# Kernel tuning notes

Measured on AMD Instinct MI355X. Metric: run time of the kernel, lower is better.

The kernel has to match this reference:

```python
import jax, jax.numpy as jnp
import numpy as np

D = 1024  # dim_context


def setup_inputs() -> dict:
    key = jax.random.key(0)
    k1, k2, k3, k4, k5 = jax.random.split(key, 5)
    B, T = 32, 2048
    hidden = jax.random.normal(k1, (B, D), dtype=jnp.float32)
    encoder_outputs = jax.random.normal(k2, (B, T, D), dtype=jnp.float32)
    # nn.Linear(2D, D): weight [D, 2D], bias [D]
    lim = 1.0 / np.sqrt(2 * D)
    W = jax.random.uniform(k3, (D, 2 * D), minval=-lim, maxval=lim, dtype=jnp.float32)
    b = jax.random.uniform(k4, (D,), minval=-lim, maxval=lim, dtype=jnp.float32)
    stdv = 1.0 / np.sqrt(D)
    v = jax.random.uniform(k5, (D,), minval=-stdv, maxval=stdv, dtype=jnp.float32)
    return {"hidden": hidden, "encoder_outputs": encoder_outputs, "W": W, "b": b, "v": v}


def reference(hidden, encoder_outputs, W, b, v):
    # hidden: [B, D]; encoder_outputs: [B, T, D]
    B, T, Dm = encoder_outputs.shape
    h = jnp.broadcast_to(hidden[:, None, :], (B, T, Dm))      # repeat over T
    attn_inputs = jnp.concatenate([h, encoder_outputs], axis=2)  # [B, T, 2D]
    energy = jax.nn.relu(jnp.einsum('btk,dk->btd', attn_inputs, W) + b)  # [B, T, D]
    scores = jnp.einsum('btd,d->bt', energy, v)                # [B, T]
    # softmax over dim=1 (time axis), then unsqueeze(1)
    return jax.nn.softmax(scores, axis=1)[:, None, :]          # [B, 1, T]
```

## Files before the change

### kernel.cpp

```cpp
#include <hip/hip_runtime.h>
#include <cstdint>


#define GLOBAL_AS __attribute__((address_space(1)))
#define LDS_AS    __attribute__((address_space(3)))

typedef __bf16 bf16x8 __attribute__((ext_vector_type(8)));
typedef float  f32x4  __attribute__((ext_vector_type(4)));

__device__ __forceinline__ unsigned int f2bf(float x) {
    unsigned int u = __builtin_bit_cast(unsigned int, x);
    u += 0x7fffu + ((u >> 16) & 1u);
    return u >> 16;
}

__global__ __launch_bounds__(256) void k_convert_enc(const float4* __restrict__ in,
                                                     uint4* __restrict__ out) {
    size_t idx = (size_t)blockIdx.x * 256 + threadIdx.x;
    float4 f0 = in[idx * 2];
    float4 f1 = in[idx * 2 + 1];
    uint4 o;
    o.x = f2bf(f0.x) | (f2bf(f0.y) << 16);
    o.y = f2bf(f0.z) | (f2bf(f0.w) << 16);
    o.z = f2bf(f1.x) | (f2bf(f1.y) << 16);
    o.w = f2bf(f1.z) | (f2bf(f1.w) << 16);
    out[idx] = o;
}

__global__ __launch_bounds__(256) void k_convert_we(const float* __restrict__ W,
                                                    uint2* __restrict__ out) {
    int idx = blockIdx.x * 256 + threadIdx.x;
    int i = idx * 4;
    int n = i >> 10, k = i & 1023;
    const float4 f = *(const float4*)(W + (size_t)n * 2048 + 1024 + k);
    uint2 o;
    o.x = f2bf(f.x) | (f2bf(f.y) << 16);
    o.y = f2bf(f.z) | (f2bf(f.w) << 16);
    out[idx] = o;
}

__global__ __launch_bounds__(256) void k_hidden_proj(const float* __restrict__ hidden,
                                                     const float* __restrict__ W,
                                                     const float* __restrict__ bias,
                                                     float* __restrict__ u) {
    __shared__ float wrow[1024];
    __shared__ float red[256];
    const int tid = threadIdx.x, d = blockIdx.x;
    ((float4*)wrow)[tid] = ((const float4*)(W + (size_t)d * 2048))[tid];
    __syncthreads();
    const int b = tid & 31, kc = tid >> 5;
    const float* h = hidden + b * 1024 + kc * 128;
    const float* w = wrow + kc * 128;
    float acc = 0.f;
    #pragma unroll 8
    for (int i = 0; i < 128; i += 4) {
        float4 hv = *(const float4*)(h + i);
        acc += w[i] * hv.x + w[i + 1] * hv.y + w[i + 2] * hv.z + w[i + 3] * hv.w;
    }
    red[tid] = acc;
    __syncthreads();
    if (tid < 32) {
        float s = 0.f;
        #pragma unroll
        for (int j = 0; j < 8; j++) s += red[j * 32 + tid];
        u[tid * 1024 + d] = s + bias[d];
    }
}


#define STAGE_A(S, h, kk) do {                                                          \
    __builtin_amdgcn_global_load_lds(                                                   \
        (GLOBAL_AS void*)(size_t)(Ab + arow0 + (kk) + (h) * 32),                        \
        (LDS_AS void*)(&As[S][h][c0 * 512]), 16, 0, 0);                                 \
    __builtin_amdgcn_global_load_lds(                                                   \
        (GLOBAL_AS void*)(size_t)(Ab + arow1 + (kk) + (h) * 32),                        \
        (LDS_AS void*)(&As[S][h][c0 * 512 + 512]), 16, 0, 0);                           \
} while (0)

#define STAGE_B(S, h, kk, nbn) do {                                                     \
    __builtin_amdgcn_global_load_lds(                                                   \
        (GLOBAL_AS void*)(size_t)(Bw + (size_t)(nbn) * 262144 + brow0 + (kk) + (h) * 32), \
        (LDS_AS void*)(&Bs[S][h][c0 * 512]), 16, 0, 0);                                 \
    __builtin_amdgcn_global_load_lds(                                                   \
        (GLOBAL_AS void*)(size_t)(Bw + (size_t)(nbn) * 262144 + brow1 + (kk) + (h) * 32), \
        (LDS_AS void*)(&Bs[S][h][c0 * 512 + 512]), 16, 0, 0);                           \
} while (0)

#define PHASE_MFMA(jp)                                                                  \
    __builtin_amdgcn_s_barrier();                                                       \
    asm volatile("s_waitcnt lgkmcnt(0)" ::: "memory");                                  \
    __builtin_amdgcn_sched_barrier(0);                                                  \
    __builtin_amdgcn_s_setprio(1);                                                      \
    _Pragma("unroll")                                                                   \
    for (int i = 0; i < 8; i++) {                                                       \
        acc[i][2 * (jp)]     = __builtin_amdgcn_mfma_f32_16x16x32_bf16(                 \
            afr[i], bfr[0], acc[i][2 * (jp)], 0, 0, 0);                                 \
        acc[i][2 * (jp) + 1] = __builtin_amdgcn_mfma_f32_16x16x32_bf16(                 \
            afr[i], bfr[1], acc[i][2 * (jp) + 1], 0, 0, 0);                             \
    }                                                                                   \
    __builtin_amdgcn_s_setprio(0);                                                      \
    __builtin_amdgcn_s_barrier();

#define TILE(C, S, kst, nbn) do {                                                       \
    {                                                               \
        const unsigned short* Ap = As[C][0];                                            \
        const unsigned short* Bp = Bs[C][0];                                            \
        _Pragma("unroll")                                                               \
        for (int i = 0; i < 8; i++) afr[i] = *(const bf16x8*)(Ap + aBase + i * 512);    \
        bfr[0] = *(const bf16x8*)(Bp + bBase);                                          \
        bfr[1] = *(const bf16x8*)(Bp + bBase + 512);                                    \
        STAGE_A(S, 0, kst);                                                             \
        PHASE_MFMA(0)                                                                   \
    }                                                                                   \
    {                                                               \
        const unsigned short* Bp = Bs[C][0];                                            \
        bfr[0] = *(const bf16x8*)(Bp + bBase + 1024);                                   \
        bfr[1] = *(const bf16x8*)(Bp + bBase + 1536);                                   \
        STAGE_B(S, 0, kst, nbn);                                                        \
        asm volatile("s_waitcnt vmcnt(4)" ::: "memory");                                \
        PHASE_MFMA(1)                                                                   \
    }                                                                                   \
    {                                                               \
        const unsigned short* Ap = As[C][1];                                            \
        const unsigned short* Bp = Bs[C][1];                                            \
        _Pragma("unroll")                                                               \
        for (int i = 0; i < 8; i++) afr[i] = *(const bf16x8*)(Ap + aBase + i * 512);    \
        bfr[0] = *(const bf16x8*)(Bp + bBase);                                          \
        bfr[1] = *(const bf16x8*)(Bp + bBase + 512);                                    \
        STAGE_A(S, 1, kst);                                                             \
        PHASE_MFMA(0)                                                                   \
    }                                                                                   \
    {                                                               \
        const unsigned short* Bp = Bs[C][1];                                            \
        bfr[0] = *(const bf16x8*)(Bp + bBase + 1024);                                   \
        bfr[1] = *(const bf16x8*)(Bp + bBase + 1536);                                   \
        STAGE_B(S, 1, kst, nbn);                                                        \
        asm volatile("s_waitcnt vmcnt(4)" ::: "memory");                                \
        PHASE_MFMA(1)                                                                   \
    }                                                                                   \
} while (0)

__global__ __launch_bounds__(512, 2) void k_gemm_score(
        const unsigned short* __restrict__ Ab,
        const unsigned short* __restrict__ Bw,
        const float* __restrict__ u,
        const float* __restrict__ v,
        float* __restrict__ scores) {
    __shared__ __align__(16) unsigned short As[2][2][8192];
    __shared__ __align__(16) unsigned short Bs[2][2][8192];
    __shared__ float red[4][256];

    const int tid  = threadIdx.x;
    const int wave = tid >> 6;
    const int lane = tid & 63;
    const int mb   = blockIdx.x;
    const int wm = wave & 1, wn = wave >> 1;
    const int q = lane >> 4, cl = lane & 15;
    const int bidx = mb >> 3;

    const int perm  = (q ^ ((cl >> 1) & 3)) << 3;
    const int aBase = (wm * 128 + cl) * 32 + perm;
    const int bBase = (wn * 64 + cl) * 32 + perm;

    const int c0 = wave * 2;
    const int g8 = (((lane & 3) ^ ((lane >> 3) & 3)) << 3);
    const int rowA0 = c0 * 16 + (lane >> 2);
    const size_t arow0 = (size_t)(mb * 256 + rowA0) * 1024 + g8;
    const size_t arow1 = arow0 + 16 * 1024;
    const size_t brow0 = (size_t)rowA0 * 1024 + g8;
    const size_t brow1 = brow0 + 16 * 1024;

    f32x4 acc[8][4];
    float sacc[8][4];
    bf16x8 afr[8], bfr[2];
    #pragma unroll
    for (int i = 0; i < 8; i++)
        #pragma unroll
        for (int r = 0; r < 4; r++) sacc[i][r] = 0.f;

    STAGE_A(0, 0, 0);
    STAGE_B(0, 0, 0, 0);
    STAGE_A(0, 1, 0);
    STAGE_B(0, 1, 0, 0);
    asm volatile("s_waitcnt vmcnt(4)" ::: "memory");
    __builtin_amdgcn_s_barrier();

    for (int p = 0; p < 4; p++) {
        #pragma unroll
        for (int i = 0; i < 8; i++)
            #pragma unroll
            for (int j = 0; j < 4; j++) acc[i][j] = (f32x4){0.f, 0.f, 0.f, 0.f};

        for (int it = 0; it < 8; it++) {
            const int k1 = (2 * it + 1) * 64;
            TILE(0, 1, k1, p);
            const int last = (it == 7);
            const int k2  = last ? 0 : (2 * it + 2) * 64;
            const int nb2 = last ? ((p < 3) ? p + 1 : 3) : p;
            TILE(1, 0, k2, nb2);
        }

        float vv[4], uu[4];
        #pragma unroll
        for (int j = 0; j < 4; j++) {
            int n = p * 256 + wn * 64 + j * 16 + cl;
            vv[j] = v[n];
            uu[j] = u[bidx * 1024 + n];
        }
        #pragma unroll
        for (int i = 0; i < 8; i++)
            #pragma unroll
            for (int r = 0; r < 4; r++) {
                float s = sacc[i][r];
                #pragma unroll
                for (int j = 0; j < 4; j++)
                    s += fmaxf(acc[i][j][r] + uu[j], 0.f) * vv[j];
                sacc[i][r] = s;
            }
    }

    #pragma unroll
    for (int i = 0; i < 8; i++)
        #pragma unroll
        for (int r = 0; r < 4; r++) {
            float s = sacc[i][r];
            s += __shfl_xor(s, 1);
            s += __shfl_xor(s, 2);
            s += __shfl_xor(s, 4);
            s += __shfl_xor(s, 8);
            if (cl == 0) red[wn][wm * 128 + i * 16 + q * 4 + r] = s;
        }
    __syncthreads();
    if (tid < 256) {
        scores[(size_t)mb * 256 + tid] =
            red[0][tid] + red[1][tid] + red[2][tid] + red[3][tid];
    }
}

__global__ __launch_bounds__(256) void k_softmax(const float* __restrict__ scores,
                                                 float* __restrict__ out) {
    __shared__ float red[4];
    int b = blockIdx.x;
    int t0 = threadIdx.x;
    int wave = threadIdx.x >> 6, lane = threadIdx.x & 63;
    const float* s0 = scores + b * 2048;
    float vals[8];
    float lmax = -1e30f;
    #pragma unroll
    for (int i = 0; i < 8; i++) {
        int t = t0 + i * 256;
        vals[i] = s0[t];
        lmax = fmaxf(lmax, vals[i]);
    }
    for (int o = 32; o > 0; o >>= 1) lmax = fmaxf(lmax, __shfl_xor(lmax, o));
    if (lane == 0) red[wave] = lmax;
    __syncthreads();
    float gmax = fmaxf(fmaxf(red[0], red[1]), fmaxf(red[2], red[3]));
    float lsum = 0.f;
    #pragma unroll
    for (int i = 0; i < 8; i++) {
        vals[i] = expf(vals[i] - gmax);
        lsum += vals[i];
    }
    for (int o = 32; o > 0; o >>= 1) lsum += __shfl_xor(lsum, o);
    __syncthreads();
    if (lane == 0) red[wave] = lsum;
    __syncthreads();
    float inv = 1.0f / (red[0] + red[1] + red[2] + red[3]);
    #pragma unroll
    for (int i = 0; i < 8; i++) out[b * 2048 + t0 + i * 256] = vals[i] * inv;
}

extern "C" void kernel_launch(void* const* d_in, const int* in_sizes, int n_in,
                              void* d_out, int out_size, void* d_ws, size_t ws_size,
                              hipStream_t stream) {
    const float* hidden = (const float*)d_in[0];
    const float* enc    = (const float*)d_in[1];
    const float* W      = (const float*)d_in[2];
    const float* bias   = (const float*)d_in[3];
    const float* v      = (const float*)d_in[4];
    float* out = (float*)d_out;

    char* ws = (char*)d_ws;
    unsigned short* encb = (unsigned short*)ws;
    unsigned short* Web  = (unsigned short*)(ws + 134217728);
    float* u      = (float*)(ws + 134217728 + 2097152);
    float* scores = (float*)(ws + 134217728 + 2097152 + 131072);

    k_convert_enc<<<32768, 256, 0, stream>>>((const float4*)enc, (uint4*)encb);
    k_convert_we<<<1024, 256, 0, stream>>>(W, (uint2*)Web);
    k_hidden_proj<<<1024, 256, 0, stream>>>(hidden, W, bias, u);
    k_gemm_score<<<256, 512, 0, stream>>>(encb, Web, u, v, scores);
    k_softmax<<<32, 256, 0, stream>>>(scores, out);
}
```

Before: 575.7 us.

## Split GEMM N dimension across blocks and reduce partial scores in softmax

The GEMM-score kernel previously looped over four 256-wide N chunks inside each block (256 blocks). It now launches 1024 blocks, each handling one M tile and one N chunk, with a block-index swizzle that groups blocks by N chunk. Each block writes partial scores to a 4x buffer, and the softmax kernel sums the four partials. This aims to fill the GPU better (256 blocks was only about one wave on many CUs), at the cost of re-reading A tiles four times and extra partial-score traffic.

```diff
diff --git a/kernel.cpp b/kernel.cpp
--- a/kernel.cpp
+++ b/kernel.cpp
@@ -77,12 +77,12 @@
         (LDS_AS void*)(&As[S][h][c0 * 512 + 512]), 16, 0, 0);                           \
 } while (0)
 
-#define STAGE_B(S, h, kk, nbn) do {                                                     \
-    __builtin_amdgcn_global_load_lds(                                                   \
-        (GLOBAL_AS void*)(size_t)(Bw + (size_t)(nbn) * 262144 + brow0 + (kk) + (h) * 32), \
+#define STAGE_B(S, h, kk) do {                                                          \
+    __builtin_amdgcn_global_load_lds(                                                   \
+        (GLOBAL_AS void*)(size_t)(Bbase + brow0 + (kk) + (h) * 32),                     \
         (LDS_AS void*)(&Bs[S][h][c0 * 512]), 16, 0, 0);                                 \
     __builtin_amdgcn_global_load_lds(                                                   \
-        (GLOBAL_AS void*)(size_t)(Bw + (size_t)(nbn) * 262144 + brow1 + (kk) + (h) * 32), \
+        (GLOBAL_AS void*)(size_t)(Bbase + brow1 + (kk) + (h) * 32),                     \
         (LDS_AS void*)(&Bs[S][h][c0 * 512 + 512]), 16, 0, 0);                           \
 } while (0)
 
@@ -101,7 +101,7 @@
     __builtin_amdgcn_s_setprio(0);                                                      \
     __builtin_amdgcn_s_barrier();
 
-#define TILE(C, S, kst, nbn) do {                                                       \
+#define TILE(C, S, kst) do {                                                            \
     {                                                               \
         const unsigned short* Ap = As[C][0];                                            \
         const unsigned short* Bp = Bs[C][0];                                            \
@@ -116,7 +116,7 @@
         const unsigned short* Bp = Bs[C][0];                                            \
         bfr[0] = *(const bf16x8*)(Bp + bBase + 1024);                                   \
         bfr[1] = *(const bf16x8*)(Bp + bBase + 1536);                                   \
-        STAGE_B(S, 0, kst, nbn);                                                        \
+        STAGE_B(S, 0, kst);                                                             \
         asm volatile("s_waitcnt vmcnt(4)" ::: "memory");                                \
         PHASE_MFMA(1)                                                                   \
     }                                                                                   \
@@ -134,7 +134,7 @@
         const unsigned short* Bp = Bs[C][1];                                            \
         bfr[0] = *(const bf16x8*)(Bp + bBase + 1024);                                   \
         bfr[1] = *(const bf16x8*)(Bp + bBase + 1536);                                   \
-        STAGE_B(S, 1, kst, nbn);                                                        \
+        STAGE_B(S, 1, kst);                                                             \
         asm volatile("s_waitcnt vmcnt(4)" ::: "memory");                                \
         PHASE_MFMA(1)                                                                   \
     }                                                                                   \
@@ -145,7 +145,7 @@
         const unsigned short* __restrict__ Bw,
         const float* __restrict__ u,
         const float* __restrict__ v,
-        float* __restrict__ scores) {
+        float* __restrict__ scores4) {
     __shared__ __align__(16) unsigned short As[2][2][8192];
     __shared__ __align__(16) unsigned short Bs[2][2][8192];
     __shared__ float red[4][256];
@@ -153,7 +153,10 @@
     const int tid  = threadIdx.x;
     const int wave = tid >> 6;
     const int lane = tid & 63;
-    const int mb   = blockIdx.x;
+    const int bid  = blockIdx.x;
+    const int lg   = (bid & 7) * 128 + (bid >> 3);
+    const int mb   = lg >> 2;
+    const int nb   = lg & 3;
     const int wm = wave & 1, wn = wave >> 1;
     const int q = lane >> 4, cl = lane & 15;
     const int bidx = mb >> 3;
@@ -169,61 +172,44 @@
     const size_t arow1 = arow0 + 16 * 1024;
     const size_t brow0 = (size_t)rowA0 * 1024 + g8;
     const size_t brow1 = brow0 + 16 * 1024;
+    const unsigned short* Bbase = Bw + (size_t)nb * 262144;
 
     f32x4 acc[8][4];
-    float sacc[8][4];
     bf16x8 afr[8], bfr[2];
     #pragma unroll
     for (int i = 0; i < 8; i++)
         #pragma unroll
-        for (int r = 0; r < 4; r++) sacc[i][r] = 0.f;
+        for (int j = 0; j < 4; j++) acc[i][j] = (f32x4){0.f, 0.f, 0.f, 0.f};
 
     STAGE_A(0, 0, 0);
-    STAGE_B(0, 0, 0, 0);
+    STAGE_B(0, 0, 0);
     STAGE_A(0, 1, 0);
-    STAGE_B(0, 1, 0, 0);
+    STAGE_B(0, 1, 0);
     asm volatile("s_waitcnt vmcnt(4)" ::: "memory");
     __builtin_amdgcn_s_barrier();
 
-    for (int p = 0; p < 4; p++) {
-        #pragma unroll
-        for (int i = 0; i < 8; i++)
-            #pragma unroll
-            for (int j = 0; j < 4; j++) acc[i][j] = (f32x4){0.f, 0.f, 0.f, 0.f};
-
-        for (int it = 0; it < 8; it++) {
-            const int k1 = (2 * it + 1) * 64;
-            TILE(0, 1, k1, p);
-            const int last = (it == 7);
-            const int k2  = last ? 0 : (2 * it + 2) * 64;
-            const int nb2 = last ? ((p < 3) ? p + 1 : 3) : p;
-            TILE(1, 0, k2, nb2);
-        }
-
-        float vv[4], uu[4];
-        #pragma unroll
-        for (int j = 0; j < 4; j++) {
-            int n = p * 256 + wn * 64 + j * 16 + cl;
-            vv[j] = v[n];
-            uu[j] = u[bidx * 1024 + n];
-        }
-        #pragma unroll
-        for (int i = 0; i < 8; i++)
-            #pragma unroll
-            for (int r = 0; r < 4; r++) {
-                float s = sacc[i][r];
-                #pragma unroll
-                for (int j = 0; j < 4; j++)
-                    s += fmaxf(acc[i][j][r] + uu[j], 0.f) * vv[j];
-                sacc[i][r] = s;
-            }
-    }
-
+    for (int it = 0; it < 8; it++) {
+        const int k1 = (2 * it + 1) * 64;
+        TILE(0, 1, k1);
+        const int k2 = (it == 7) ? 0 : (2 * it + 2) * 64;
+        TILE(1, 0, k2);
+    }
+
+    float vv[4], uu[4];
+    #pragma unroll
+    for (int j = 0; j < 4; j++) {
+        int n = nb * 256 + wn * 64 + j * 16 + cl;
+        vv[j] = v[n];
+        uu[j] = u[bidx * 1024 + n];
+    }
     #pragma unroll
     for (int i = 0; i < 8; i++)
         #pragma unroll
         for (int r = 0; r < 4; r++) {
-            float s = sacc[i][r];
+            float s = 0.f;
+            #pragma unroll
+            for (int j = 0; j < 4; j++)
+                s += fmaxf(acc[i][j][r] + uu[j], 0.f) * vv[j];
             s += __shfl_xor(s, 1);
             s += __shfl_xor(s, 2);
             s += __shfl_xor(s, 4);
@@ -232,24 +218,24 @@
         }
     __syncthreads();
     if (tid < 256) {
-        scores[(size_t)mb * 256 + tid] =
+        scores4[(size_t)nb * 65536 + mb * 256 + tid] =
             red[0][tid] + red[1][tid] + red[2][tid] + red[3][tid];
     }
 }
 
-__global__ __launch_bounds__(256) void k_softmax(const float* __restrict__ scores,
+__global__ __launch_bounds__(256) void k_softmax(const float* __restrict__ scores4,
                                                  float* __restrict__ out) {
     __shared__ float red[4];
     int b = blockIdx.x;
     int t0 = threadIdx.x;
     int wave = threadIdx.x >> 6, lane = threadIdx.x & 63;
-    const float* s0 = scores + b * 2048;
+    const float* s0 = scores4 + b * 2048;
     float vals[8];
     float lmax = -1e30f;
     #pragma unroll
     for (int i = 0; i < 8; i++) {
         int t = t0 + i * 256;
-        vals[i] = s0[t];
+        vals[i] = s0[t] + s0[65536 + t] + s0[131072 + t] + s0[196608 + t];
         lmax = fmaxf(lmax, vals[i]);
     }
     for (int o = 32; o > 0; o >>= 1) lmax = fmaxf(lmax, __shfl_xor(lmax, o));
@@ -284,12 +270,12 @@
     char* ws = (char*)d_ws;
     unsigned short* encb = (unsigned short*)ws;
     unsigned short* Web  = (unsigned short*)(ws + 134217728);
-    float* u      = (float*)(ws + 134217728 + 2097152);
-    float* scores = (float*)(ws + 134217728 + 2097152 + 131072);
+    float* u       = (float*)(ws + 134217728 + 2097152);
+    float* scores4 = (float*)(ws + 134217728 + 2097152 + 131072);
 
     k_convert_enc<<<32768, 256, 0, stream>>>((const float4*)enc, (uint4*)encb);
     k_convert_we<<<1024, 256, 0, stream>>>(W, (uint2*)Web);
     k_hidden_proj<<<1024, 256, 0, stream>>>(hidden, W, bias, u);
-    k_gemm_score<<<256, 512, 0, stream>>>(encb, Web, u, v, scores);
-    k_softmax<<<32, 256, 0, stream>>>(scores, out);
-}
+    k_gemm_score<<<1024, 512, 0, stream>>>(encb, Web, u, v, scores4);
+    k_softmax<<<32, 256, 0, stream>>>(scores4, out);
+}
```

Result: no change. 570.3 us (-0.9%).
